# Kernel tuning notes

Measured on AMD Instinct MI355X. Metric: run time of the kernel, lower is better.

## Reference

```python
import jax, jax.numpy as jnp
import numpy as np

HARDNESS = 5.0

def setup_inputs() -> dict:
    key = jax.random.key(0)
    k1, k2 = jax.random.split(key)
    x = jax.random.normal(k1, (64, 8, 32, 32, 16), dtype=jnp.float32)
    ref = jax.random.normal(k2, (64, 16), dtype=jnp.float32)
    return {"input": x, "ref": ref}

def reference(input, ref):
    # Squared L2 distance from every element vector (last dim) to every codeword,
    x2 = jnp.sum(input * input, axis=-1)                      # (D1,D2,D3,D4)
    r2 = jnp.sum(ref * ref, axis=-1)                          # (M,)
    cross = jnp.einsum('abcde,me->mabcd', input, ref)         # (M,D1,D2,D3,D4)
    sq_l2 = x2[None] - 2.0 * cross + r2[:, None, None, None, None]
    # Softmax over codebook axis with -hardness temperature (dim=0 in torch).
    y = jax.nn.softmax(-HARDNESS * sq_l2, axis=0)             # (M,D1,D2,D3,D4)
    # Weighted combination of codewords.
    z = jnp.einsum('mabcd,me->abcde', y, ref)                 # (D1..D5)
    return z
```

## Files before the change

kernel.cpp:

```cpp
#include <hip/hip_runtime.h>
#include <math.h>

#define CB_M 64
#define CB_D 16
#define HARD 5.0f
#define LOG2E 1.44269504088896340736f
#define LDS_STRIDE 68

typedef __attribute__((ext_vector_type(8))) short bf16x8;
typedef __attribute__((ext_vector_type(4))) float f32x4;

#if __has_builtin(__builtin_amdgcn_exp2f)
#define EXP2F(x) __builtin_amdgcn_exp2f(x)
#else
#define EXP2F(x) exp2f(x)
#endif

__device__ __forceinline__ ushort f2bf(float f) {
    unsigned u = __float_as_uint(f);
    u += 0x7fffu + ((u >> 16) & 1u);
    return (ushort)(u >> 16);
}
__device__ __forceinline__ float bf2f(ushort h) {
    return __uint_as_float(((unsigned)h) << 16);
}

__global__ void stq_prep(const float* __restrict__ ref, char* __restrict__ ws) {
    float*  bias   = (float*)(ws);
    ushort* rs_hi  = (ushort*)(ws + 256);
    ushort* rs_lo  = (ushort*)(ws + 2304);
    ushort* rzT_hi = (ushort*)(ws + 4352);
    ushort* rzT_lo = (ushort*)(ws + 6400);

    int m = threadIdx.x;
    if (m >= CB_M) return;
    float r[CB_D];
    float r2 = 0.0f;
    for (int j = 0; j < CB_D; ++j) { r[j] = ref[m * CB_D + j]; r2 += r[j] * r[j]; }
    bias[m] = -(HARD * LOG2E) * r2;
    const float s = 2.0f * HARD * LOG2E;
    for (int j = 0; j < CB_D; ++j) {
        float v = s * r[j];
        ushort h = f2bf(v);
        rs_hi[m * CB_D + j] = h;
        rs_lo[m * CB_D + j] = f2bf(v - bf2f(h));
        ushort zh = f2bf(r[j]);
        rzT_hi[j * CB_M + m] = zh;
        rzT_lo[j * CB_M + m] = f2bf(r[j] - bf2f(zh));
    }
}

__global__ __launch_bounds__(256, 3) void stq_main(const float* __restrict__ x,
                                                   const char* __restrict__ ws,
                                                   float* __restrict__ out,
                                                   int ntiles) {
    const float*  bias   = (const float*)(ws);
    const ushort* rs_hi  = (const ushort*)(ws + 256);
    const ushort* rs_lo  = (const ushort*)(ws + 2304);
    const ushort* rzT_hi = (const ushort*)(ws + 4352);
    const ushort* rzT_lo = (const ushort*)(ws + 6400);

    __shared__ float slds[4][16 * LDS_STRIDE];

    const int lane = threadIdx.x & 63;
    const int wid  = threadIdx.x >> 6;
    const int i = lane & 15;
    const int c = lane >> 4;
    float* S = slds[wid];

    bf16x8 BsH[4], BsL[4];
    float biasv[4];
#pragma unroll
    for (int t = 0; t < 4; ++t) {
        biasv[t] = bias[16 * t + i];
        BsH[t] = *(const bf16x8*)(rs_hi + (16 * t + i) * CB_D + (c & 1) * 8);
        BsL[t] = *(const bf16x8*)(rs_lo + (16 * t + i) * CB_D + (c & 1) * 8);
    }
    bf16x8 BzH0 = *(const bf16x8*)(rzT_hi + i * CB_M + c * 8);
    bf16x8 BzH1 = *(const bf16x8*)(rzT_hi + i * CB_M + 32 + c * 8);
    bf16x8 BzL0 = *(const bf16x8*)(rzT_lo + i * CB_M + c * 8);
    bf16x8 BzL1 = *(const bf16x8*)(rzT_lo + i * CB_M + 32 + c * 8);

    const int nwaves = gridDim.x * 4;
    for (int tile = blockIdx.x * 4 + wid; tile < ntiles; tile += nwaves) {
        const int rowbase = tile * 16;

        const float* xp = x + (size_t)(rowbase + i) * CB_D + (c & 1) * 8;
        f32x4 xa = *(const f32x4*)xp;
        f32x4 xb = *(const f32x4*)(xp + 4);
        float xf[8] = {xa.x, xa.y, xa.z, xa.w, xb.x, xb.y, xb.z, xb.w};
        const bool wantlo = (c >= 2);
        bf16x8 A;
#pragma unroll
        for (int j = 0; j < 8; ++j) {
            ushort h = f2bf(xf[j]);
            ushort l = f2bf(xf[j] - bf2f(h));
            A[j] = (short)(wantlo ? l : h);
        }

        f32x4 acc[4];
#pragma unroll
        for (int t = 0; t < 4; ++t) {
            f32x4 cinit = {biasv[t], biasv[t], biasv[t], biasv[t]};
            acc[t] = __builtin_amdgcn_mfma_f32_16x16x32_bf16(A, BsH[t], cinit, 0, 0, 0);
            acc[t] = __builtin_amdgcn_mfma_f32_16x16x32_bf16(A, BsL[t], acc[t], 0, 0, 0);
        }

#pragma unroll
        for (int t = 0; t < 4; ++t)
#pragma unroll
            for (int r = 0; r < 4; ++r)
                S[(4 * c + r) * LDS_STRIDE + i + 16 * t] = acc[t][r];

        float sv[16];
        {
            const f32x4* p0 = (const f32x4*)(S + i * LDS_STRIDE + c * 8);
            const f32x4* p1 = (const f32x4*)(S + i * LDS_STRIDE + 32 + c * 8);
            f32x4 a0 = p0[0], a1 = p0[1], b0 = p1[0], b1 = p1[1];
            sv[0]=a0.x; sv[1]=a0.y; sv[2]=a0.z; sv[3]=a0.w;
            sv[4]=a1.x; sv[5]=a1.y; sv[6]=a1.z; sv[7]=a1.w;
            sv[8]=b0.x; sv[9]=b0.y; sv[10]=b0.z; sv[11]=b0.w;
            sv[12]=b1.x; sv[13]=b1.y; sv[14]=b1.z; sv[15]=b1.w;
        }

        float lmax = sv[0];
#pragma unroll
        for (int j = 1; j < 16; ++j) lmax = fmaxf(lmax, sv[j]);
        lmax = fmaxf(lmax, __shfl_xor(lmax, 16, 64));
        lmax = fmaxf(lmax, __shfl_xor(lmax, 32, 64));

        float e[16];
        float lsum = 0.0f;
#pragma unroll
        for (int j = 0; j < 16; ++j) { e[j] = EXP2F(sv[j] - lmax); lsum += e[j]; }
        lsum += __shfl_xor(lsum, 16, 64);
        lsum += __shfl_xor(lsum, 32, 64);
        const float inv = 1.0f / lsum;

        bf16x8 P1, P2;
#pragma unroll
        for (int j = 0; j < 8; ++j) {
            P1[j] = (short)f2bf(e[j] * inv);
            P2[j] = (short)f2bf(e[8 + j] * inv);
        }

        f32x4 cz = {0.0f, 0.0f, 0.0f, 0.0f};
        cz = __builtin_amdgcn_mfma_f32_16x16x32_bf16(P1, BzH0, cz, 0, 0, 0);
        cz = __builtin_amdgcn_mfma_f32_16x16x32_bf16(P2, BzH1, cz, 0, 0, 0);
        cz = __builtin_amdgcn_mfma_f32_16x16x32_bf16(P1, BzL0, cz, 0, 0, 0);
        cz = __builtin_amdgcn_mfma_f32_16x16x32_bf16(P2, BzL1, cz, 0, 0, 0);

#pragma unroll
        for (int r = 0; r < 4; ++r)
            out[(size_t)(rowbase + 4 * c + r) * CB_D + i] = cz[r];
    }
}

extern "C" void kernel_launch(void* const* d_in, const int* in_sizes, int n_in,
                              void* d_out, int out_size, void* d_ws, size_t ws_size,
                              hipStream_t stream) {
    const float* x   = (const float*)d_in[0];
    const float* ref = (const float*)d_in[1];
    float* out = (float*)d_out;
    char* ws = (char*)d_ws;

    const int nvec = in_sizes[0] / CB_D;
    const int ntiles = nvec / 16;

    stq_prep<<<1, 64, 0, stream>>>(ref, ws);
    stq_main<<<1024, 256, 0, stream>>>(x, ws, out, ntiles);
}
```

Baseline: 95.87 us.

## Fuse codebook prep into main kernel, prefetch next tile, cheaper bf16 packing

Removes the separate prep kernel launch: each block now builds the codebook tables in shared memory and syncs before the main loop. The x loads for the next tile are software-prefetched one iteration ahead. The bf16 split of x and of the softmax weights now uses truncation with round-half-up and byte-permute packing, and the reciprocal uses the hardware rcp builtin, cutting ALU work. Launch bounds drop to 2 blocks per SIMD, and the per-block prep costs redundant work across 1024 blocks, with slightly different rounding.

```diff
diff --git a/kernel.cpp b/kernel.cpp
--- a/kernel.cpp
+++ b/kernel.cpp
@@ -5,10 +5,11 @@
 #define CB_D 16
 #define HARD 5.0f
 #define LOG2E 1.44269504088896340736f
-#define LDS_STRIDE 68
+#define SSTRIDE 68
 
 typedef __attribute__((ext_vector_type(8))) short bf16x8;
 typedef __attribute__((ext_vector_type(4))) float f32x4;
+typedef __attribute__((ext_vector_type(4))) int   i32x4;
 
 #if __has_builtin(__builtin_amdgcn_exp2f)
 #define EXP2F(x) __builtin_amdgcn_exp2f(x)
@@ -16,7 +17,13 @@
 #define EXP2F(x) exp2f(x)
 #endif
 
-__device__ __forceinline__ ushort f2bf(float f) {
+#if __has_builtin(__builtin_amdgcn_rcpf)
+#define RCPF(x) __builtin_amdgcn_rcpf(x)
+#else
+#define RCPF(x) (1.0f / (x))
+#endif
+
+__device__ __forceinline__ ushort f2bf_rne(float f) {
     unsigned u = __float_as_uint(f);
     u += 0x7fffu + ((u >> 16) & 1u);
     return (ushort)(u >> 16);
@@ -24,85 +31,113 @@
 __device__ __forceinline__ float bf2f(ushort h) {
     return __uint_as_float(((unsigned)h) << 16);
 }
-
-__global__ void stq_prep(const float* __restrict__ ref, char* __restrict__ ws) {
-    float*  bias   = (float*)(ws);
-    ushort* rs_hi  = (ushort*)(ws + 256);
-    ushort* rs_lo  = (ushort*)(ws + 2304);
-    ushort* rzT_hi = (ushort*)(ws + 4352);
-    ushort* rzT_lo = (ushort*)(ws + 6400);
-
-    int m = threadIdx.x;
-    if (m >= CB_M) return;
-    float r[CB_D];
-    float r2 = 0.0f;
-    for (int j = 0; j < CB_D; ++j) { r[j] = ref[m * CB_D + j]; r2 += r[j] * r[j]; }
-    bias[m] = -(HARD * LOG2E) * r2;
-    const float s = 2.0f * HARD * LOG2E;
-    for (int j = 0; j < CB_D; ++j) {
-        float v = s * r[j];
-        ushort h = f2bf(v);
-        rs_hi[m * CB_D + j] = h;
-        rs_lo[m * CB_D + j] = f2bf(v - bf2f(h));
-        ushort zh = f2bf(r[j]);
-        rzT_hi[j * CB_M + m] = zh;
-        rzT_lo[j * CB_M + m] = f2bf(r[j] - bf2f(zh));
-    }
-}
-
-__global__ __launch_bounds__(256, 3) void stq_main(const float* __restrict__ x,
-                                                   const char* __restrict__ ws,
+__device__ __forceinline__ int pk(float a, float b) {
+    return (int)__builtin_amdgcn_perm(__float_as_uint(a), __float_as_uint(b), 0x07060302u);
+}
+__device__ __forceinline__ float rnd(float a) {
+    return __uint_as_float(__float_as_uint(a) + 0x8000u);
+}
+__device__ __forceinline__ float hi_trunc(float a) {
+    return __uint_as_float(__float_as_uint(a) & 0xffff0000u);
+}
+
+__global__ __launch_bounds__(256, 2) void stq_main(const float* __restrict__ x,
+                                                   const float* __restrict__ ref,
                                                    float* __restrict__ out,
                                                    int ntiles) {
-    const float*  bias   = (const float*)(ws);
-    const ushort* rs_hi  = (const ushort*)(ws + 256);
-    const ushort* rs_lo  = (const ushort*)(ws + 2304);
-    const ushort* rzT_hi = (const ushort*)(ws + 4352);
-    const ushort* rzT_lo = (const ushort*)(ws + 6400);
-
-    __shared__ float slds[4][16 * LDS_STRIDE];
-
-    const int lane = threadIdx.x & 63;
-    const int wid  = threadIdx.x >> 6;
+    __shared__ __align__(16) float  cb_bias[CB_M];
+    __shared__ __align__(16) ushort cb_rs_hi[CB_M][CB_D];
+    __shared__ __align__(16) ushort cb_rs_lo[CB_M][CB_D];
+    __shared__ __align__(16) ushort cb_rzT_hi[CB_D][CB_M];
+    __shared__ __align__(16) ushort cb_rzT_lo[CB_D][CB_M];
+    __shared__ __align__(16) float  slds[4][16 * SSTRIDE];
+
+    const int tid = threadIdx.x;
+
+    if (tid < CB_M) {
+        const f32x4* rp = (const f32x4*)(ref + tid * CB_D);
+        f32x4 q0 = rp[0], q1 = rp[1], q2 = rp[2], q3 = rp[3];
+        float r[CB_D] = {q0.x,q0.y,q0.z,q0.w, q1.x,q1.y,q1.z,q1.w,
+                         q2.x,q2.y,q2.z,q2.w, q3.x,q3.y,q3.z,q3.w};
+        float r2 = 0.0f;
+#pragma unroll
+        for (int j = 0; j < CB_D; ++j) r2 += r[j] * r[j];
+        cb_bias[tid] = -(HARD * LOG2E) * r2;
+        const float s = 2.0f * HARD * LOG2E;
+#pragma unroll
+        for (int j = 0; j < CB_D; ++j) {
+            float v = s * r[j];
+            ushort h = f2bf_rne(v);
+            cb_rs_hi[tid][j] = h;
+            cb_rs_lo[tid][j] = f2bf_rne(v - bf2f(h));
+            ushort zh = f2bf_rne(r[j]);
+            cb_rzT_hi[j][tid] = zh;
+            cb_rzT_lo[j][tid] = f2bf_rne(r[j] - bf2f(zh));
+        }
+    }
+    __syncthreads();
+
+    const int lane = tid & 63;
+    const int wid  = tid >> 6;
     const int i = lane & 15;
     const int c = lane >> 4;
+    const bool wantlo = (c >= 2);
     float* S = slds[wid];
 
     bf16x8 BsH[4], BsL[4];
-    float biasv[4];
+    f32x4  cinit[4];
 #pragma unroll
     for (int t = 0; t < 4; ++t) {
-        biasv[t] = bias[16 * t + i];
-        BsH[t] = *(const bf16x8*)(rs_hi + (16 * t + i) * CB_D + (c & 1) * 8);
-        BsL[t] = *(const bf16x8*)(rs_lo + (16 * t + i) * CB_D + (c & 1) * 8);
-    }
-    bf16x8 BzH0 = *(const bf16x8*)(rzT_hi + i * CB_M + c * 8);
-    bf16x8 BzH1 = *(const bf16x8*)(rzT_hi + i * CB_M + 32 + c * 8);
-    bf16x8 BzL0 = *(const bf16x8*)(rzT_lo + i * CB_M + c * 8);
-    bf16x8 BzL1 = *(const bf16x8*)(rzT_lo + i * CB_M + 32 + c * 8);
+        float b = cb_bias[16 * t + i];
+        cinit[t] = (f32x4){b, b, b, b};
+        BsH[t] = *(const bf16x8*)&cb_rs_hi[16 * t + i][(c & 1) * 8];
+        BsL[t] = *(const bf16x8*)&cb_rs_lo[16 * t + i][(c & 1) * 8];
+    }
+    bf16x8 BzH0 = *(const bf16x8*)&cb_rzT_hi[i][c * 8];
+    bf16x8 BzH1 = *(const bf16x8*)&cb_rzT_hi[i][32 + c * 8];
+    bf16x8 BzL0 = *(const bf16x8*)&cb_rzT_lo[i][c * 8];
+    bf16x8 BzL1 = *(const bf16x8*)&cb_rzT_lo[i][32 + c * 8];
 
     const int nwaves = gridDim.x * 4;
-    for (int tile = blockIdx.x * 4 + wid; tile < ntiles; tile += nwaves) {
-        const int rowbase = tile * 16;
-
-        const float* xp = x + (size_t)(rowbase + i) * CB_D + (c & 1) * 8;
-        f32x4 xa = *(const f32x4*)xp;
-        f32x4 xb = *(const f32x4*)(xp + 4);
-        float xf[8] = {xa.x, xa.y, xa.z, xa.w, xb.x, xb.y, xb.z, xb.w};
-        const bool wantlo = (c >= 2);
-        bf16x8 A;
-#pragma unroll
-        for (int j = 0; j < 8; ++j) {
-            ushort h = f2bf(xf[j]);
-            ushort l = f2bf(xf[j] - bf2f(h));
-            A[j] = (short)(wantlo ? l : h);
-        }
+    int tile = blockIdx.x * 4 + wid;
+
+    f32x4 nxa, nxb;
+    {
+        const float* xp = x + ((size_t)tile * 16 + i) * CB_D + (c & 1) * 8;
+        nxa = *(const f32x4*)xp;
+        nxb = *(const f32x4*)(xp + 4);
+    }
+
+#pragma unroll 1
+    for (; tile < ntiles; tile += nwaves) {
+        f32x4 xa = nxa, xb = nxb;
+        const int nt = tile + nwaves;
+        if (nt < ntiles) {
+            const float* xp = x + ((size_t)nt * 16 + i) * CB_D + (c & 1) * 8;
+            nxa = *(const f32x4*)xp;
+            nxb = *(const f32x4*)(xp + 4);
+        }
+
+        i32x4 Ahi, Alo;
+        Ahi.x = pk(xa.y, xa.x); Ahi.y = pk(xa.w, xa.z);
+        Ahi.z = pk(xb.y, xb.x); Ahi.w = pk(xb.w, xb.z);
+        float l0 = xa.x - hi_trunc(xa.x), l1 = xa.y - hi_trunc(xa.y);
+        float l2 = xa.z - hi_trunc(xa.z), l3 = xa.w - hi_trunc(xa.w);
+        float l4 = xb.x - hi_trunc(xb.x), l5 = xb.y - hi_trunc(xb.y);
+        float l6 = xb.z - hi_trunc(xb.z), l7 = xb.w - hi_trunc(xb.w);
+        Alo.x = pk(rnd(l1), rnd(l0)); Alo.y = pk(rnd(l3), rnd(l2));
+        Alo.z = pk(rnd(l5), rnd(l4)); Alo.w = pk(rnd(l7), rnd(l6));
+        i32x4 Ai;
+        Ai.x = wantlo ? Alo.x : Ahi.x;
+        Ai.y = wantlo ? Alo.y : Ahi.y;
+        Ai.z = wantlo ? Alo.z : Ahi.z;
+        Ai.w = wantlo ? Alo.w : Ahi.w;
+        bf16x8 A = __builtin_bit_cast(bf16x8, Ai);
 
         f32x4 acc[4];
 #pragma unroll
         for (int t = 0; t < 4; ++t) {
-            f32x4 cinit = {biasv[t], biasv[t], biasv[t], biasv[t]};
-            acc[t] = __builtin_amdgcn_mfma_f32_16x16x32_bf16(A, BsH[t], cinit, 0, 0, 0);
+            acc[t] = __builtin_amdgcn_mfma_f32_16x16x32_bf16(A, BsH[t], cinit[t], 0, 0, 0);
             acc[t] = __builtin_amdgcn_mfma_f32_16x16x32_bf16(A, BsL[t], acc[t], 0, 0, 0);
         }
 
@@ -110,12 +145,12 @@
         for (int t = 0; t < 4; ++t)
 #pragma unroll
             for (int r = 0; r < 4; ++r)
-                S[(4 * c + r) * LDS_STRIDE + i + 16 * t] = acc[t][r];
+                S[(4 * c + r) * SSTRIDE + i + 16 * t] = acc[t][r];
 
         float sv[16];
         {
-            const f32x4* p0 = (const f32x4*)(S + i * LDS_STRIDE + c * 8);
-            const f32x4* p1 = (const f32x4*)(S + i * LDS_STRIDE + 32 + c * 8);
+            const f32x4* p0 = (const f32x4*)(S + i * SSTRIDE + c * 8);
+            const f32x4* p1 = (const f32x4*)(S + i * SSTRIDE + 32 + c * 8);
             f32x4 a0 = p0[0], a1 = p0[1], b0 = p1[0], b1 = p1[1];
             sv[0]=a0.x; sv[1]=a0.y; sv[2]=a0.z; sv[3]=a0.w;
             sv[4]=a1.x; sv[5]=a1.y; sv[6]=a1.z; sv[7]=a1.w;
@@ -135,14 +170,19 @@
         for (int j = 0; j < 16; ++j) { e[j] = EXP2F(sv[j] - lmax); lsum += e[j]; }
         lsum += __shfl_xor(lsum, 16, 64);
         lsum += __shfl_xor(lsum, 32, 64);
-        const float inv = 1.0f / lsum;
-
-        bf16x8 P1, P2;
-#pragma unroll
-        for (int j = 0; j < 8; ++j) {
-            P1[j] = (short)f2bf(e[j] * inv);
-            P2[j] = (short)f2bf(e[8 + j] * inv);
-        }
+        const float inv = RCPF(lsum);
+
+        i32x4 P1i, P2i;
+        P1i.x = pk(rnd(e[1] * inv),  rnd(e[0] * inv));
+        P1i.y = pk(rnd(e[3] * inv),  rnd(e[2] * inv));
+        P1i.z = pk(rnd(e[5] * inv),  rnd(e[4] * inv));
+        P1i.w = pk(rnd(e[7] * inv),  rnd(e[6] * inv));
+        P2i.x = pk(rnd(e[9] * inv),  rnd(e[8] * inv));
+        P2i.y = pk(rnd(e[11] * inv), rnd(e[10] * inv));
+        P2i.z = pk(rnd(e[13] * inv), rnd(e[12] * inv));
+        P2i.w = pk(rnd(e[15] * inv), rnd(e[14] * inv));
+        bf16x8 P1 = __builtin_bit_cast(bf16x8, P1i);
+        bf16x8 P2 = __builtin_bit_cast(bf16x8, P2i);
 
         f32x4 cz = {0.0f, 0.0f, 0.0f, 0.0f};
         cz = __builtin_amdgcn_mfma_f32_16x16x32_bf16(P1, BzH0, cz, 0, 0, 0);
@@ -150,6 +190,7 @@
         cz = __builtin_amdgcn_mfma_f32_16x16x32_bf16(P1, BzL0, cz, 0, 0, 0);
         cz = __builtin_amdgcn_mfma_f32_16x16x32_bf16(P2, BzL1, cz, 0, 0, 0);
 
+        const int rowbase = tile * 16;
 #pragma unroll
         for (int r = 0; r < 4; ++r)
             out[(size_t)(rowbase + 4 * c + r) * CB_D + i] = cz[r];
@@ -162,11 +203,9 @@
     const float* x   = (const float*)d_in[0];
     const float* ref = (const float*)d_in[1];
     float* out = (float*)d_out;
-    char* ws = (char*)d_ws;
 
     const int nvec = in_sizes[0] / CB_D;
     const int ntiles = nvec / 16;
 
-    stq_prep<<<1, 64, 0, stream>>>(ref, ws);
-    stq_main<<<1024, 256, 0, stream>>>(x, ws, out, ntiles);
-}
+    stq_main<<<1024, 256, 0, stream>>>(x, ref, out, ntiles);
+}
```

Result: faster. 89.70 us (-6.4%).
